# Optimization experiments

Hardware: AMD Instinct MI355X
Metric: run time of the kernel (lower is better)

Reference implementation:

```python
import jax, jax.numpy as jnp
import numpy as np

NUM_FEATURES = 256
NUM_HEADS = 8
HEAD_SIZE = NUM_FEATURES // NUM_HEADS  # 32
N_AGENTS = 8
B = 32
SEQ = 64


def setup_inputs() -> dict:
    key = jax.random.key(0)
    ks = jax.random.split(key, 6)
    s = 0.02
    x = jax.random.normal(ks[0], (N_AGENTS * B, NUM_FEATURES, SEQ), dtype=jnp.float32)
    Wq = jax.random.normal(ks[1], (NUM_HEADS, NUM_FEATURES, HEAD_SIZE), dtype=jnp.float32) * s
    Wk = jax.random.normal(ks[2], (NUM_HEADS, NUM_FEATURES, HEAD_SIZE), dtype=jnp.float32) * s
    Wv = jax.random.normal(ks[3], (NUM_HEADS, NUM_FEATURES, HEAD_SIZE), dtype=jnp.float32) * s
    Wp = jax.random.normal(ks[4], (NUM_FEATURES, NUM_FEATURES), dtype=jnp.float32) * s
    bp = jnp.zeros((NUM_FEATURES,), dtype=jnp.float32)
    return {"x": x, "Wq": Wq, "Wk": Wk, "Wv": Wv, "Wp": Wp, "bp": bp, "n_agents": N_AGENTS}


def reference(x, Wq, Wk, Wv, Wp, bp, n_agents):
    # x: (n_agents*b, f, h)
    b_total, f, h = x.shape
    b = b_total // n_agents
    # reshape + rearrange 'n b f h -> n b h f'  (t = token axis of length h)
    xs = x.reshape(n_agents, b, f, h).transpose(0, 1, 3, 2)  # (n, b, t, f)
    # All heads at once: per-head linear projections (no bias)
    q = jnp.einsum('nbtf,Hfd->Hnbtd', xs, Wq)
    k = jnp.einsum('nbtf,Hfd->Hnbtd', xs, Wk)
    v = jnp.einsum('nbtf,Hfd->Hnbtd', xs, Wv)
    # all-pairs agent attention: i = key agent, j = query agent
    scale = f ** (-0.5)  # source scales by num_features, not head_size
    scores = jnp.einsum('Hjbtd,Hibsd->Hijbts', q, k) * scale  # (H,n,n,b,t,s)
    attn = jax.nn.softmax(scores, axis=-1)
    # weighted values, then sum over key-agent axis i
    out = jnp.einsum('Hijbts,Hibsd->Hjbtd', attn, v)  # (H,n,b,t,d)
    # concat heads on last dim (head 0 first), matching torch.cat
    y = jnp.moveaxis(out, 0, 3).reshape(n_agents, b, h, f)  # (n,b,t,H*d)
    # output projection (dropout is identity at eval / p=0)
    y = jnp.einsum('nbtf,gf->nbtg', y, Wp) + bp
    # rearrange 'n b h f -> n b f h' then merge agents into batch
    y = y.transpose(0, 1, 3, 2).reshape(n_agents * b, f, h)
    return y
```

## Files before the change

kernel.cpp:

```cpp
#include <hip/hip_runtime.h>

#define F   256
#define T   64
#define NH  8
#define D   32
#define NA  8
#define NBB 32

typedef unsigned short ushortT;
typedef unsigned int   uintT;

typedef short bf16x8 __attribute__((ext_vector_type(8)));
typedef float f32x4  __attribute__((ext_vector_type(4)));

__device__ __forceinline__ float bf2f(ushortT u) {
    union { uintT i; float f; } c; c.i = ((uintT)u) << 16; return c.f;
}
__device__ __forceinline__ ushortT f2bf(float f) {
    union { float f; uintT u; } c; c.f = f;
    uintT u = c.u;
    uintT r = u + 0x7fffu + ((u >> 16) & 1u);
    return (ushortT)(r >> 16);
}

__device__ __forceinline__ int detect_isbf16(const void* xraw) {
    const uintT* w = (const uintT*)xraw;
    int bad = 0;
    for (int k = 0; k < 128; ++k) {
        uintT v = w[k];
        uintT e0 = (v >> 7)  & 0xffu;
        uintT e1 = (v >> 23) & 0xffu;
        bad += (e0 > 131u) + (e1 > 131u);
    }
    return bad == 0 ? 1 : 0;
}

__device__ __forceinline__ ushortT cvt_elem(const void* p, size_t i, bool isbf) {
    return isbf ? ((const ushortT*)p)[i] : f2bf(((const float*)p)[i]);
}

__device__ __forceinline__ void packc(const f32x4 v, float scale, uintT& u0, uintT& u1) {
    u0 = (uintT)f2bf(v[0] * scale) | ((uintT)f2bf(v[1] * scale) << 16);
    u1 = (uintT)f2bf(v[2] * scale) | ((uintT)f2bf(v[3] * scale) << 16);
}

__device__ __forceinline__ bf16x8 build_frag(uintT u0a, uintT u1a, uintT u0b, uintT u1b,
                                             int sl0, int sl1, bool hi) {
    union { uintT u[4]; bf16x8 v; } r;
    uintT x0a = (uintT)__shfl((int)u0a, sl0), x0b = (uintT)__shfl((int)u0b, sl0);
    uintT x1a = (uintT)__shfl((int)u1a, sl0), x1b = (uintT)__shfl((int)u1b, sl0);
    uintT x2a = (uintT)__shfl((int)u0a, sl1), x2b = (uintT)__shfl((int)u0b, sl1);
    uintT x3a = (uintT)__shfl((int)u1a, sl1), x3b = (uintT)__shfl((int)u1b, sl1);
    r.u[0] = hi ? x0b : x0a;
    r.u[1] = hi ? x1b : x1a;
    r.u[2] = hi ? x2b : x2a;
    r.u[3] = hi ? x3b : x3a;
    return r.v;
}

__device__ __forceinline__ int xposU(int t, int f) {
    return t * 256 + ((((f >> 3) ^ (t & 31)) * 8) | (f & 7));
}
#define FRAGPOS(t_, ks_, quad_) \
    ((t_) * 256 + ((((4 * (ks_) + (quad_)) ^ ((t_) & 31)) * 8)))

template <int NT>
__device__ __forceinline__ void stage_xT(const void* x, int nb, ushortT* xs,
                                         bool isbf, int tid) {
    int t = tid & 63;
    int g0 = tid >> 6;
    const int GP = NT / 64;
    #pragma unroll
    for (int it = 0; it < 64 / GP; ++it) {
        int g = g0 + it * GP;
        float v0, v1, v2, v3;
        if (isbf) {
            const ushortT* xp = (const ushortT*)x + (size_t)nb * (F * T) + (size_t)g * 4 * T + t;
            v0 = bf2f(xp[0]); v1 = bf2f(xp[T]); v2 = bf2f(xp[2 * T]); v3 = bf2f(xp[3 * T]);
        } else {
            const float* xp = (const float*)x + (size_t)nb * (F * T) + (size_t)g * 4 * T + t;
            v0 = xp[0]; v1 = xp[T]; v2 = xp[2 * T]; v3 = xp[3 * T];
        }
        uintT lo = (uintT)f2bf(v0) | ((uintT)f2bf(v1) << 16);
        uintT hi2 = (uintT)f2bf(v2) | ((uintT)f2bf(v3) << 16);
        *(uint2*)&xs[xposU(t, g * 4)] = make_uint2(lo, hi2);
    }
}


__global__ __launch_bounds__(256) void wprep_kernel(const void* __restrict__ Wq,
                                                    const void* __restrict__ Wk,
                                                    const void* __restrict__ Wv,
                                                    const void* __restrict__ x,
                                                    ushortT* __restrict__ Wt) {
    __shared__ int sflag;
    if (threadIdx.x == 0) sflag = detect_isbf16(x);
    __syncthreads();
    bool isbf = sflag != 0;

    int base = (blockIdx.x * 256 + threadIdx.x) * 8;
    int cp = base >> 8, f0 = base & 255;
    int qkv = cp >> 8, c = cp & 255, hh = c >> 5, d = c & 31;
    const void* W = (qkv == 0) ? Wq : (qkv == 1) ? Wk : Wv;

    ushortT tmp[8];
    #pragma unroll
    for (int jj = 0; jj < 8; ++jj)
        tmp[jj] = cvt_elem(W, (size_t)(hh * F + f0 + jj) * D + d, isbf);
    *(uint4*)&Wt[base] = *(const uint4*)tmp;
}

__global__ __launch_bounds__(256) void qkv_kernel(const void* __restrict__ x,
                                                  const ushortT* __restrict__ Wt,
                                                  ushortT* __restrict__ Kws,
                                                  ushortT* __restrict__ Vws) {
    int nb = blockIdx.x, half = blockIdx.y;
    __shared__ __align__(16) ushortT xs[T * F];
    __shared__ int sflag;
    int tid = threadIdx.x;
    if (tid == 0) sflag = detect_isbf16(x);
    __syncthreads();
    bool isbf = sflag != 0;
    stage_xT<256>(x, nb, xs, isbf, tid);
    __syncthreads();

    int w = tid >> 6, lane = tid & 63, l15 = lane & 15, quad = lane >> 4;
    int rowbase = 256 + 256 * half + 64 * w;

    f32x4 acc[4][4];
    #pragma unroll
    for (int a = 0; a < 4; ++a)
        #pragma unroll
        for (int c = 0; c < 4; ++c) acc[a][c] = (f32x4){0.f, 0.f, 0.f, 0.f};

    #pragma unroll
    for (int ks = 0; ks < 8; ++ks) {
        bf16x8 Bfr[4];
        #pragma unroll
        for (int nt = 0; nt < 4; ++nt) {
            int t = 16 * nt + l15;
            Bfr[nt] = *(const bf16x8*)&xs[FRAGPOS(t, ks, quad)];
        }
        #pragma unroll
        for (int mt = 0; mt < 4; ++mt) {
            bf16x8 Afr = *(const bf16x8*)(Wt +
                (size_t)(rowbase + 16 * mt + l15) * 256 + ks * 32 + quad * 8);
            #pragma unroll
            for (int nt = 0; nt < 4; ++nt)
                acc[mt][nt] = __builtin_amdgcn_mfma_f32_16x16x32_bf16(Afr, Bfr[nt],
                                                                      acc[mt][nt], 0, 0, 0);
        }
    }

    #pragma unroll
    for (int mt = 0; mt < 4; ++mt) {
        int rel = 64 * w + 16 * mt + 4 * quad;
        int hh = rel >> 5, db = rel & 31;
        #pragma unroll
        for (int nt = 0; nt < 4; ++nt) {
            int t = 16 * nt + l15;
            f32x4 v = acc[mt][nt];
            if (half == 0) {
                ushortT* dst = Kws + ((size_t)(nb * NH + hh) * T + t) * D + db;
                uintT lo = (uintT)f2bf(v[0]) | ((uintT)f2bf(v[1]) << 16);
                uintT hi2 = (uintT)f2bf(v[2]) | ((uintT)f2bf(v[3]) << 16);
                *(uint2*)dst = make_uint2(lo, hi2);
            } else {
                #pragma unroll
                for (int r = 0; r < 4; ++r)
                    Vws[((size_t)(nb * NH + hh) * D + db + r) * T + t] = f2bf(v[r]);
            }
        }
    }
}

__global__ __launch_bounds__(512, 2) void attn_kernel(const void* __restrict__ x,
                                                      const ushortT* __restrict__ Wt,
                                                      const ushortT* __restrict__ Kws,
                                                      const ushortT* __restrict__ Vws,
                                                      const void* __restrict__ Wp,
                                                      const void* __restrict__ bp,
                                                      void* __restrict__ outp) {
    __shared__ __align__(16) ushortT xs[T * F];
    __shared__ float bpf[F];
    __shared__ int sflag;

    int tid = threadIdx.x;
    int b = blockIdx.x, j = blockIdx.y;
    int nbj = j * NBB + b;

    if (tid == 0) sflag = detect_isbf16(x);
    __syncthreads();
    bool isbf = sflag != 0;
    stage_xT<512>(x, nbj, xs, isbf, tid);
    if (tid < 256)
        bpf[tid] = isbf ? bf2f(((const ushortT*)bp)[tid]) : ((const float*)bp)[tid];
    __syncthreads();

    int h = tid >> 6, lane = tid & 63, l15 = lane & 15, quad = lane >> 4;
    bool hi = quad >= 2;
    int sl0 = l15 + 32 * (quad & 1), sl1 = sl0 + 16;

    bf16x8 qf[4];
    {
        f32x4 qacc[2][4];
        #pragma unroll
        for (int mt = 0; mt < 2; ++mt)
            #pragma unroll
            for (int nt = 0; nt < 4; ++nt) qacc[mt][nt] = (f32x4){0.f, 0.f, 0.f, 0.f};
        #pragma unroll
        for (int ks = 0; ks < 8; ++ks) {
            bf16x8 xf[4];
            #pragma unroll
            for (int nt = 0; nt < 4; ++nt) {
                int t = 16 * nt + l15;
                xf[nt] = *(const bf16x8*)&xs[FRAGPOS(t, ks, quad)];
            }
            #pragma unroll
            for (int mt = 0; mt < 2; ++mt) {
                bf16x8 Aw = *(const bf16x8*)(Wt +
                    (size_t)(32 * h + 16 * mt + l15) * 256 + ks * 32 + quad * 8);
                #pragma unroll
                for (int nt = 0; nt < 4; ++nt)
                    qacc[mt][nt] = __builtin_amdgcn_mfma_f32_16x16x32_bf16(
                        Aw, xf[nt], qacc[mt][nt], 0, 0, 0);
            }
        }
        #pragma unroll
        for (int tt = 0; tt < 4; ++tt) {
            uintT a0, a1, b0, b1;
            packc(qacc[0][tt], 0.0625f, a0, a1);
            packc(qacc[1][tt], 0.0625f, b0, b1);
            qf[tt] = build_frag(a0, a1, b0, b1, sl0, sl1, hi);
        }
    }

    f32x4 oacc[2][4];
    #pragma unroll
    for (int mt = 0; mt < 2; ++mt)
        #pragma unroll
        for (int tt = 0; tt < 4; ++tt) oacc[mt][tt] = (f32x4){0.f, 0.f, 0.f, 0.f};

    #pragma unroll
    for (int i = 0; i < NA; ++i) {
        int nbi = i * NBB + b;
        const ushortT* Kb = Kws + (size_t)(nbi * NH + h) * T * D;
        const ushortT* Vb = Vws + (size_t)(nbi * NH + h) * D * T;

        bf16x8 kf[4], vf[2][2];
        #pragma unroll
        for (int st = 0; st < 4; ++st)
            kf[st] = *(const bf16x8*)(Kb + (16 * st + l15) * D + quad * 8);
        #pragma unroll
        for (int mt = 0; mt < 2; ++mt)
            #pragma unroll
            for (int kx = 0; kx < 2; ++kx)
                vf[mt][kx] = *(const bf16x8*)(Vb + (16 * mt + l15) * T + kx * 32 + quad * 8);

        float psum[4] = {0.f, 0.f, 0.f, 0.f};
        uintT pu0[4][4], pu1[4][4];
        #pragma unroll
        for (int st = 0; st < 4; ++st) {
            f32x4 s4[4];
            #pragma unroll
            for (int tt = 0; tt < 4; ++tt)
                s4[tt] = __builtin_amdgcn_mfma_f32_16x16x32_bf16(
                    kf[st], qf[tt], (f32x4){0.f, 0.f, 0.f, 0.f}, 0, 0, 0);
            #pragma unroll
            for (int tt = 0; tt < 4; ++tt) {
                #pragma unroll
                for (int r = 0; r < 4; ++r) {
                    float e = __expf(s4[tt][r]);
                    s4[tt][r] = e;
                    psum[tt] += e;
                }
                packc(s4[tt], 1.f, pu0[st][tt], pu1[st][tt]);
            }
        }
        float inv[4];
        #pragma unroll
        for (int tt = 0; tt < 4; ++tt) {
            float s = psum[tt];
            s += __shfl_xor(s, 16);
            s += __shfl_xor(s, 32);
            inv[tt] = 1.0f / s;
        }

        f32x4 pv[2][4];
        #pragma unroll
        for (int mt = 0; mt < 2; ++mt)
            #pragma unroll
            for (int tt = 0; tt < 4; ++tt) pv[mt][tt] = (f32x4){0.f, 0.f, 0.f, 0.f};
        #pragma unroll
        for (int kx = 0; kx < 2; ++kx) {
            #pragma unroll
            for (int tt = 0; tt < 4; ++tt) {
                bf16x8 pf = build_frag(pu0[2 * kx][tt], pu1[2 * kx][tt],
                                       pu0[2 * kx + 1][tt], pu1[2 * kx + 1][tt],
                                       sl0, sl1, hi);
                #pragma unroll
                for (int mt = 0; mt < 2; ++mt)
                    pv[mt][tt] = __builtin_amdgcn_mfma_f32_16x16x32_bf16(
                        vf[mt][kx], pf, pv[mt][tt], 0, 0, 0);
            }
        }
        #pragma unroll
        for (int mt = 0; mt < 2; ++mt)
            #pragma unroll
            for (int tt = 0; tt < 4; ++tt)
                #pragma unroll
                for (int r = 0; r < 4; ++r)
                    oacc[mt][tt][r] = fmaf(inv[tt], pv[mt][tt][r], oacc[mt][tt][r]);
    }

    __syncthreads();
    #pragma unroll
    for (int mt = 0; mt < 2; ++mt)
        #pragma unroll
        for (int tt = 0; tt < 4; ++tt) {
            int t = 16 * tt + l15;
            int cb = 32 * h + 16 * mt + 4 * quad;
            uintT u0, u1;
            packc(oacc[mt][tt], 1.f, u0, u1);
            *(uint2*)&xs[xposU(t, cb)] = make_uint2(u0, u1);
        }
    __syncthreads();

    f32x4 cacc[2][4];
    #pragma unroll
    for (int a = 0; a < 2; ++a)
        #pragma unroll
        for (int c = 0; c < 4; ++c) cacc[a][c] = (f32x4){0.f, 0.f, 0.f, 0.f};

    #pragma unroll
    for (int ks = 0; ks < 8; ++ks) {
        bf16x8 yb[4];
        #pragma unroll
        for (int nt = 0; nt < 4; ++nt) {
            int t = 16 * nt + l15;
            yb[nt] = *(const bf16x8*)&xs[FRAGPOS(t, ks, quad)];
        }
        #pragma unroll
        for (int m2 = 0; m2 < 2; ++m2) {
            int g = 16 * (2 * h + m2) + l15;
            bf16x8 wf;
            if (isbf) {
                wf = *(const bf16x8*)((const ushortT*)Wp + (size_t)g * 256 +
                                      ks * 32 + quad * 8);
            } else {
                const float* wr = (const float*)Wp + (size_t)g * 256 + ks * 32 + quad * 8;
                float4 w0 = *(const float4*)wr;
                float4 w1 = *(const float4*)(wr + 4);
                union { ushortT s[8]; bf16x8 v; } wt;
                wt.s[0] = f2bf(w0.x); wt.s[1] = f2bf(w0.y);
                wt.s[2] = f2bf(w0.z); wt.s[3] = f2bf(w0.w);
                wt.s[4] = f2bf(w1.x); wt.s[5] = f2bf(w1.y);
                wt.s[6] = f2bf(w1.z); wt.s[7] = f2bf(w1.w);
                wf = wt.v;
            }
            #pragma unroll
            for (int nt = 0; nt < 4; ++nt)
                cacc[m2][nt] = __builtin_amdgcn_mfma_f32_16x16x32_bf16(
                    wf, yb[nt], cacc[m2][nt], 0, 0, 0);
        }
    }

    #pragma unroll
    for (int m2 = 0; m2 < 2; ++m2)
        #pragma unroll
        for (int nt = 0; nt < 4; ++nt) {
            int t = 16 * nt + l15;
            #pragma unroll
            for (int r = 0; r < 4; ++r) {
                int g = 16 * (2 * h + m2) + 4 * quad + r;
                float val = cacc[m2][nt][r] + bpf[g];
                if (isbf)
                    ((ushortT*)outp)[(size_t)nbj * F * T + g * T + t] = f2bf(val);
                else
                    ((float*)outp)[(size_t)nbj * F * T + g * T + t] = val;
            }
        }
}

__device__ __forceinline__ float tof(ushortT u) { return bf2f(u); }
__device__ __forceinline__ float tof(float f)   { return f; }

__device__ __forceinline__ void stage_x(const void* x, size_t nb, ushortT* sX,
                                        bool isbf, int tid) {
    if (isbf) {
        const int4* xg = (const int4*)((const ushortT*)x + nb * (F * T));
        int4* xl = (int4*)sX;
        for (int kk = tid; kk < F * T / 8; kk += 512) xl[kk] = xg[kk];
    } else {
        const float4* xg = (const float4*)((const float*)x + nb * (F * T));
        for (int kk = tid; kk < F * T / 4; kk += 512) {
            float4 v = xg[kk];
            int o = kk * 4;
            sX[o + 0] = f2bf(v.x); sX[o + 1] = f2bf(v.y);
            sX[o + 2] = f2bf(v.z); sX[o + 3] = f2bf(v.w);
        }
    }
}

template <typename WT>
__device__ __forceinline__ void q_proj(const WT* __restrict__ W, const ushortT* sX,
                                       ushortT* dst, int c, int t0) {
    float acc[32];
    #pragma unroll
    for (int m = 0; m < 32; ++m) acc[m] = 0.f;
    for (int f = 0; f < F; ++f) {
        float w = tof(W[f * D]);
        const ushortT* xr = &sX[f * T + t0];
        #pragma unroll
        for (int m = 0; m < 32; ++m) acc[m] = fmaf(bf2f(xr[m]), w, acc[m]);
    }
    #pragma unroll
    for (int m = 0; m < 32; ++m) dst[(t0 + m) * F + c] = f2bf(acc[m]);
}

template <typename WT>
__device__ __forceinline__ void kv_proj(const WT* __restrict__ WK, const WT* __restrict__ WV,
                                        const ushortT* sX, ushortT* sK, ushortT* sV,
                                        int c, int t0) {
    float ak[32], av[32];
    #pragma unroll
    for (int m = 0; m < 32; ++m) { ak[m] = 0.f; av[m] = 0.f; }
    for (int f = 0; f < F; ++f) {
        float wk = tof(WK[f * D]);
        float wv = tof(WV[f * D]);
        const ushortT* xr = &sX[f * T + t0];
        #pragma unroll
        for (int m = 0; m < 32; ++m) {
            float xv = bf2f(xr[m]);
            ak[m] = fmaf(xv, wk, ak[m]);
            av[m] = fmaf(xv, wv, av[m]);
        }
    }
    #pragma unroll
    for (int m = 0; m < 32; ++m) {
        sK[(t0 + m) * F + c] = f2bf(ak[m]);
        sV[(t0 + m) * F + c] = f2bf(av[m]);
    }
}

__global__ __launch_bounds__(512) void fused_kernel(const void* __restrict__ x,
                                                    const void* __restrict__ Wq,
                                                    const void* __restrict__ Wk,
                                                    const void* __restrict__ Wv,
                                                    const void* __restrict__ Wp,
                                                    const void* __restrict__ bp,
                                                    void* __restrict__ outp) {
    __shared__ __align__(16) char smem[98304];
    __shared__ int sflag;
    ushortT* sX = (ushortT*)smem;
    ushortT* sK = (ushortT*)(smem + 32768);
    ushortT* sV = (ushortT*)(smem + 65536);
    float*   sO = (float*)smem;

    int tid = threadIdx.x;
    int b = blockIdx.x, j = blockIdx.y;
    size_t nbj = (size_t)j * NBB + b;

    if (tid == 0) sflag = detect_isbf16(x);
    __syncthreads();
    bool isbf = sflag != 0;

    stage_x(x, nbj, sX, isbf, tid);
    __syncthreads();

    int c = tid & 255, t0 = (tid >> 8) * 32;
    int hc = c >> 5, dc = c & 31;
    if (isbf) q_proj((const ushortT*)Wq + (size_t)hc * F * D + dc, sX, sK, c, t0);
    else      q_proj((const float*)Wq   + (size_t)hc * F * D + dc, sX, sK, c, t0);
    __syncthreads();

    int h = tid >> 6, t = tid & 63;
    float q[32], o[32];
    #pragma unroll
    for (int dd = 0; dd < 32; ++dd) { q[dd] = bf2f(sK[t * F + h * D + dd]); o[dd] = 0.f; }

    for (int i = 0; i < NA; ++i) {
        __syncthreads();
        stage_x(x, (size_t)(i * NBB + b), sX, isbf, tid);
        __syncthreads();
        if (isbf) kv_proj((const ushortT*)Wk + (size_t)hc * F * D + dc,
                          (const ushortT*)Wv + (size_t)hc * F * D + dc, sX, sK, sV, c, t0);
        else      kv_proj((const float*)Wk   + (size_t)hc * F * D + dc,
                          (const float*)Wv   + (size_t)hc * F * D + dc, sX, sK, sV, c, t0);
        __syncthreads();
        float l = 0.f;
        float oi[32];
        #pragma unroll
        for (int dd = 0; dd < 32; ++dd) oi[dd] = 0.f;
        for (int s = 0; s < T; ++s) {
            const ushortT* kr = &sK[s * F + h * D];
            float dot = 0.f;
            #pragma unroll
            for (int dd = 0; dd < 32; ++dd) dot = fmaf(q[dd], bf2f(kr[dd]), dot);
            float e = __expf(dot * 0.0625f);
            l += e;
            const ushortT* vr = &sV[s * F + h * D];
            #pragma unroll
            for (int dd = 0; dd < 32; ++dd) oi[dd] = fmaf(e, bf2f(vr[dd]), oi[dd]);
        }
        float inv = 1.0f / l;
        #pragma unroll
        for (int dd = 0; dd < 32; ++dd) o[dd] = fmaf(oi[dd], inv, o[dd]);
    }
    __syncthreads();

    #pragma unroll
    for (int dd = 0; dd < 32; ++dd) sO[(h * D + dd) * T + t] = o[dd];
    __syncthreads();

    {
        int g = tid >> 1, te0 = (tid & 1) * 32;
        float acc[32];
        #pragma unroll
        for (int m = 0; m < 32; ++m) acc[m] = 0.f;
        if (isbf) {
            const ushortT* Wrow = (const ushortT*)Wp + (size_t)g * F;
            for (int cc = 0; cc < F; ++cc) {
                float w = bf2f(Wrow[cc]);
                const float* yr = &sO[cc * T + te0];
                #pragma unroll
                for (int m = 0; m < 32; ++m) acc[m] = fmaf(yr[m], w, acc[m]);
            }
        } else {
            const float* Wrow = (const float*)Wp + (size_t)g * F;
            for (int cc = 0; cc < F; ++cc) {
                float w = Wrow[cc];
                const float* yr = &sO[cc * T + te0];
                #pragma unroll
                for (int m = 0; m < 32; ++m) acc[m] = fmaf(yr[m], w, acc[m]);
            }
        }
        float bias = isbf ? bf2f(((const ushortT*)bp)[g]) : ((const float*)bp)[g];
        if (isbf) {
            ushortT* ob = (ushortT*)outp + nbj * F * T + g * T + te0;
            #pragma unroll
            for (int m = 0; m < 32; ++m) ob[m] = f2bf(acc[m] + bias);
        } else {
            float* ob = (float*)outp + nbj * F * T + g * T + te0;
            #pragma unroll
            for (int m = 0; m < 32; ++m) ob[m] = acc[m] + bias;
        }
    }
}

extern "C" void kernel_launch(void* const* d_in, const int* in_sizes, int n_in,
                              void* d_out, int out_size, void* d_ws, size_t ws_size,
                              hipStream_t stream) {
    const void* x  = d_in[0];
    const void* Wq = d_in[1];
    const void* Wk = d_in[2];
    const void* Wv = d_in[3];
    const void* Wp = d_in[4];
    const void* bp = d_in[5];

    const size_t needA = 17170432;

    if (ws_size >= needA) {
        char* ws = (char*)d_ws;
        ushortT* Wt  = (ushortT*)(ws + 0);
        ushortT* Kws = (ushortT*)(ws + 393216);
        ushortT* Vws = (ushortT*)(ws + 8781824);

        wprep_kernel<<<dim3(96),     dim3(256), 0, stream>>>(Wq, Wk, Wv, x, Wt);
        qkv_kernel  <<<dim3(256, 2), dim3(256), 0, stream>>>(x, Wt, Kws, Vws);
        attn_kernel <<<dim3(32, 8),  dim3(512), 0, stream>>>(x, Wt, Kws, Vws, Wp, bp, d_out);
    } else {
        fused_kernel<<<dim3(32, 8), dim3(512), 0, stream>>>(x, Wq, Wk, Wv, Wp, bp, d_out);
    }
}
```

Measured before the change: 164.2 us.

## Split attention kernel across query-token halves and pre-convert Wp to bf16

```diff
diff --git a/kernel.cpp b/kernel.cpp
--- a/kernel.cpp
+++ b/kernel.cpp
@@ -64,6 +64,37 @@
 #define FRAGPOS(t_, ks_, quad_) \
     ((t_) * 256 + ((((4 * (ks_) + (quad_)) ^ ((t_) & 31)) * 8)))
 
+
+__global__ __launch_bounds__(256) void wprep_kernel(const void* __restrict__ Wq,
+                                                    const void* __restrict__ Wk,
+                                                    const void* __restrict__ Wv,
+                                                    const void* __restrict__ Wp,
+                                                    const void* __restrict__ x,
+                                                    ushortT* __restrict__ Wt) {
+    __shared__ int sflag;
+    if (threadIdx.x == 0) sflag = detect_isbf16(x);
+    __syncthreads();
+    bool isbf = sflag != 0;
+
+    int base = (blockIdx.x * 256 + threadIdx.x) * 8;
+    int cp = base >> 8, f0 = base & 255;
+
+    ushortT tmp[8];
+    if (cp < 768) {
+        int qkv = cp >> 8, c = cp & 255, hh = c >> 5, d = c & 31;
+        const void* W = (qkv == 0) ? Wq : (qkv == 1) ? Wk : Wv;
+        #pragma unroll
+        for (int jj = 0; jj < 8; ++jj)
+            tmp[jj] = cvt_elem(W, (size_t)(hh * F + f0 + jj) * D + d, isbf);
+    } else {
+        int g = cp - 768;
+        #pragma unroll
+        for (int jj = 0; jj < 8; ++jj)
+            tmp[jj] = cvt_elem(Wp, (size_t)g * F + f0 + jj, isbf);
+    }
+    *(uint4*)&Wt[base] = *(const uint4*)tmp;
+}
+
 template <int NT>
 __device__ __forceinline__ void stage_xT(const void* x, int nb, ushortT* xs,
                                          bool isbf, int tid) {
@@ -83,31 +114,8 @@
         }
         uintT lo = (uintT)f2bf(v0) | ((uintT)f2bf(v1) << 16);
         uintT hi2 = (uintT)f2bf(v2) | ((uintT)f2bf(v3) << 16);
-        *(uint2*)&xs[xposU(t, g * 4)] = make_uint2(lo, hi2);
-    }
-}
-
-
-__global__ __launch_bounds__(256) void wprep_kernel(const void* __restrict__ Wq,
-                                                    const void* __restrict__ Wk,
-                                                    const void* __restrict__ Wv,
-                                                    const void* __restrict__ x,
-                                                    ushortT* __restrict__ Wt) {
-    __shared__ int sflag;
-    if (threadIdx.x == 0) sflag = detect_isbf16(x);
-    __syncthreads();
-    bool isbf = sflag != 0;
-
-    int base = (blockIdx.x * 256 + threadIdx.x) * 8;
-    int cp = base >> 8, f0 = base & 255;
-    int qkv = cp >> 8, c = cp & 255, hh = c >> 5, d = c & 31;
-    const void* W = (qkv == 0) ? Wq : (qkv == 1) ? Wk : Wv;
-
-    ushortT tmp[8];
-    #pragma unroll
-    for (int jj = 0; jj < 8; ++jj)
-        tmp[jj] = cvt_elem(W, (size_t)(hh * F + f0 + jj) * D + d, isbf);
-    *(uint4*)&Wt[base] = *(const uint4*)tmp;
+        *(uint2*)&xs[xposU(t & 31, g * 4) + (t >> 5) * 8192] = make_uint2(lo, hi2);
+    }
 }
 
 __global__ __launch_bounds__(256) void qkv_kernel(const void* __restrict__ x,
@@ -139,7 +147,7 @@
         #pragma unroll
         for (int nt = 0; nt < 4; ++nt) {
             int t = 16 * nt + l15;
-            Bfr[nt] = *(const bf16x8*)&xs[FRAGPOS(t, ks, quad)];
+            Bfr[nt] = *(const bf16x8*)&xs[FRAGPOS(t & 31, ks, quad) + (t >> 5) * 8192];
         }
         #pragma unroll
         for (int mt = 0; mt < 4; ++mt) {
@@ -178,21 +186,41 @@
                                                       const ushortT* __restrict__ Wt,
                                                       const ushortT* __restrict__ Kws,
                                                       const ushortT* __restrict__ Vws,
-                                                      const void* __restrict__ Wp,
                                                       const void* __restrict__ bp,
                                                       void* __restrict__ outp) {
-    __shared__ __align__(16) ushortT xs[T * F];
+    __shared__ __align__(16) ushortT xs[32 * F];
     __shared__ float bpf[F];
     __shared__ int sflag;
 
     int tid = threadIdx.x;
-    int b = blockIdx.x, j = blockIdx.y;
+    int b = blockIdx.x, j = blockIdx.y, tb = blockIdx.z;
     int nbj = j * NBB + b;
 
     if (tid == 0) sflag = detect_isbf16(x);
     __syncthreads();
     bool isbf = sflag != 0;
-    stage_xT<512>(x, nbj, xs, isbf, tid);
+
+    {
+        int t = tid & 31, fg = tid >> 5;
+        int ta = tb * 32 + t;
+        #pragma unroll
+        for (int it = 0; it < 4; ++it) {
+            int f0 = (fg + 16 * it) * 4;
+            float v0, v1, v2, v3;
+            if (isbf) {
+                const ushortT* xp = (const ushortT*)x + (size_t)nbj * (F * T) +
+                                    (size_t)f0 * T + ta;
+                v0 = bf2f(xp[0]); v1 = bf2f(xp[T]); v2 = bf2f(xp[2 * T]); v3 = bf2f(xp[3 * T]);
+            } else {
+                const float* xp = (const float*)x + (size_t)nbj * (F * T) +
+                                  (size_t)f0 * T + ta;
+                v0 = xp[0]; v1 = xp[T]; v2 = xp[2 * T]; v3 = xp[3 * T];
+            }
+            uintT lo = (uintT)f2bf(v0) | ((uintT)f2bf(v1) << 16);
+            uintT hi2 = (uintT)f2bf(v2) | ((uintT)f2bf(v3) << 16);
+            *(uint2*)&xs[xposU(t, f0)] = make_uint2(lo, hi2);
+        }
+    }
     if (tid < 256)
         bpf[tid] = isbf ? bf2f(((const ushortT*)bp)[tid]) : ((const float*)bp)[tid];
     __syncthreads();
@@ -201,33 +229,31 @@
     bool hi = quad >= 2;
     int sl0 = l15 + 32 * (quad & 1), sl1 = sl0 + 16;
 
-    bf16x8 qf[4];
+    bf16x8 qf[2];
     {
-        f32x4 qacc[2][4];
+        f32x4 qacc[2][2];
         #pragma unroll
         for (int mt = 0; mt < 2; ++mt)
             #pragma unroll
-            for (int nt = 0; nt < 4; ++nt) qacc[mt][nt] = (f32x4){0.f, 0.f, 0.f, 0.f};
+            for (int nt = 0; nt < 2; ++nt) qacc[mt][nt] = (f32x4){0.f, 0.f, 0.f, 0.f};
         #pragma unroll
         for (int ks = 0; ks < 8; ++ks) {
-            bf16x8 xf[4];
-            #pragma unroll
-            for (int nt = 0; nt < 4; ++nt) {
-                int t = 16 * nt + l15;
-                xf[nt] = *(const bf16x8*)&xs[FRAGPOS(t, ks, quad)];
-            }
+            bf16x8 xf[2];
+            #pragma unroll
+            for (int nt = 0; nt < 2; ++nt)
+                xf[nt] = *(const bf16x8*)&xs[FRAGPOS(16 * nt + l15, ks, quad)];
             #pragma unroll
             for (int mt = 0; mt < 2; ++mt) {
                 bf16x8 Aw = *(const bf16x8*)(Wt +
                     (size_t)(32 * h + 16 * mt + l15) * 256 + ks * 32 + quad * 8);
                 #pragma unroll
-                for (int nt = 0; nt < 4; ++nt)
+                for (int nt = 0; nt < 2; ++nt)
                     qacc[mt][nt] = __builtin_amdgcn_mfma_f32_16x16x32_bf16(
                         Aw, xf[nt], qacc[mt][nt], 0, 0, 0);
             }
         }
         #pragma unroll
-        for (int tt = 0; tt < 4; ++tt) {
+        for (int tt = 0; tt < 2; ++tt) {
             uintT a0, a1, b0, b1;
             packc(qacc[0][tt], 0.0625f, a0, a1);
             packc(qacc[1][tt], 0.0625f, b0, b1);
@@ -235,89 +261,75 @@
         }
     }
 
-    f32x4 oacc[2][4];
+    f32x4 oacc[2][2];
     #pragma unroll
     for (int mt = 0; mt < 2; ++mt)
         #pragma unroll
-        for (int tt = 0; tt < 4; ++tt) oacc[mt][tt] = (f32x4){0.f, 0.f, 0.f, 0.f};
-
-    #pragma unroll
+        for (int tt = 0; tt < 2; ++tt) oacc[mt][tt] = (f32x4){0.f, 0.f, 0.f, 0.f};
+
     for (int i = 0; i < NA; ++i) {
         int nbi = i * NBB + b;
         const ushortT* Kb = Kws + (size_t)(nbi * NH + h) * T * D;
         const ushortT* Vb = Vws + (size_t)(nbi * NH + h) * D * T;
 
-        bf16x8 kf[4], vf[2][2];
-        #pragma unroll
-        for (int st = 0; st < 4; ++st)
-            kf[st] = *(const bf16x8*)(Kb + (16 * st + l15) * D + quad * 8);
+        float psum[2] = {0.f, 0.f};
+        f32x4 pv[2][2];
         #pragma unroll
         for (int mt = 0; mt < 2; ++mt)
             #pragma unroll
-            for (int kx = 0; kx < 2; ++kx)
-                vf[mt][kx] = *(const bf16x8*)(Vb + (16 * mt + l15) * T + kx * 32 + quad * 8);
-
-        float psum[4] = {0.f, 0.f, 0.f, 0.f};
-        uintT pu0[4][4], pu1[4][4];
-        #pragma unroll
-        for (int st = 0; st < 4; ++st) {
-            f32x4 s4[4];
-            #pragma unroll
-            for (int tt = 0; tt < 4; ++tt)
-                s4[tt] = __builtin_amdgcn_mfma_f32_16x16x32_bf16(
-                    kf[st], qf[tt], (f32x4){0.f, 0.f, 0.f, 0.f}, 0, 0, 0);
-            #pragma unroll
-            for (int tt = 0; tt < 4; ++tt) {
+            for (int tt = 0; tt < 2; ++tt) pv[mt][tt] = (f32x4){0.f, 0.f, 0.f, 0.f};
+
+        #pragma unroll
+        for (int kx = 0; kx < 2; ++kx) {
+            uintT pu0[2][2], pu1[2][2];
+            #pragma unroll
+            for (int sp = 0; sp < 2; ++sp) {
+                bf16x8 kf = *(const bf16x8*)(Kb + (16 * (2 * kx + sp) + l15) * D + quad * 8);
                 #pragma unroll
-                for (int r = 0; r < 4; ++r) {
-                    float e = __expf(s4[tt][r]);
-                    s4[tt][r] = e;
-                    psum[tt] += e;
+                for (int tt = 0; tt < 2; ++tt) {
+                    f32x4 s4 = __builtin_amdgcn_mfma_f32_16x16x32_bf16(
+                        kf, qf[tt], (f32x4){0.f, 0.f, 0.f, 0.f}, 0, 0, 0);
+                    #pragma unroll
+                    for (int r = 0; r < 4; ++r) {
+                        float e = __expf(s4[r]);
+                        s4[r] = e;
+                        psum[tt] += e;
+                    }
+                    packc(s4, 1.f, pu0[sp][tt], pu1[sp][tt]);
                 }
-                packc(s4[tt], 1.f, pu0[st][tt], pu1[st][tt]);
-            }
-        }
-        float inv[4];
-        #pragma unroll
-        for (int tt = 0; tt < 4; ++tt) {
+            }
+            bf16x8 vf0 = *(const bf16x8*)(Vb + l15 * T + kx * 32 + quad * 8);
+            bf16x8 vf1 = *(const bf16x8*)(Vb + (16 + l15) * T + kx * 32 + quad * 8);
+            #pragma unroll
+            for (int tt = 0; tt < 2; ++tt) {
+                bf16x8 pf = build_frag(pu0[0][tt], pu1[0][tt], pu0[1][tt], pu1[1][tt],
+                                       sl0, sl1, hi);
+                pv[0][tt] = __builtin_amdgcn_mfma_f32_16x16x32_bf16(
+                    vf0, pf, pv[0][tt], 0, 0, 0);
+                pv[1][tt] = __builtin_amdgcn_mfma_f32_16x16x32_bf16(
+                    vf1, pf, pv[1][tt], 0, 0, 0);
+            }
+        }
+
+        #pragma unroll
+        for (int tt = 0; tt < 2; ++tt) {
             float s = psum[tt];
             s += __shfl_xor(s, 16);
             s += __shfl_xor(s, 32);
-            inv[tt] = 1.0f / s;
-        }
-
-        f32x4 pv[2][4];
-        #pragma unroll
-        for (int mt = 0; mt < 2; ++mt)
-            #pragma unroll
-            for (int tt = 0; tt < 4; ++tt) pv[mt][tt] = (f32x4){0.f, 0.f, 0.f, 0.f};
-        #pragma unroll
-        for (int kx = 0; kx < 2; ++kx) {
-            #pragma unroll
-            for (int tt = 0; tt < 4; ++tt) {
-                bf16x8 pf = build_frag(pu0[2 * kx][tt], pu1[2 * kx][tt],
-                                       pu0[2 * kx + 1][tt], pu1[2 * kx + 1][tt],
-                                       sl0, sl1, hi);
-                #pragma unroll
-                for (int mt = 0; mt < 2; ++mt)
-                    pv[mt][tt] = __builtin_amdgcn_mfma_f32_16x16x32_bf16(
-                        vf[mt][kx], pf, pv[mt][tt], 0, 0, 0);
-            }
-        }
-        #pragma unroll
-        for (int mt = 0; mt < 2; ++mt)
-            #pragma unroll
-            for (int tt = 0; tt < 4; ++tt)
+            float inv = 1.0f / s;
+            #pragma unroll
+            for (int mt = 0; mt < 2; ++mt)
                 #pragma unroll
                 for (int r = 0; r < 4; ++r)
-                    oacc[mt][tt][r] = fmaf(inv[tt], pv[mt][tt][r], oacc[mt][tt][r]);
+                    oacc[mt][tt][r] = fmaf(inv, pv[mt][tt][r], oacc[mt][tt][r]);
+        }
     }
 
     __syncthreads();
     #pragma unroll
     for (int mt = 0; mt < 2; ++mt)
         #pragma unroll
-        for (int tt = 0; tt < 4; ++tt) {
+        for (int tt = 0; tt < 2; ++tt) {
             int t = 16 * tt + l15;
             int cb = 32 * h + 16 * mt + 4 * quad;
             uintT u0, u1;
@@ -326,40 +338,24 @@
         }
     __syncthreads();
 
-    f32x4 cacc[2][4];
+    f32x4 cacc[2][2];
     #pragma unroll
     for (int a = 0; a < 2; ++a)
         #pragma unroll
-        for (int c = 0; c < 4; ++c) cacc[a][c] = (f32x4){0.f, 0.f, 0.f, 0.f};
+        for (int c = 0; c < 2; ++c) cacc[a][c] = (f32x4){0.f, 0.f, 0.f, 0.f};
 
     #pragma unroll
     for (int ks = 0; ks < 8; ++ks) {
-        bf16x8 yb[4];
-        #pragma unroll
-        for (int nt = 0; nt < 4; ++nt) {
-            int t = 16 * nt + l15;
-            yb[nt] = *(const bf16x8*)&xs[FRAGPOS(t, ks, quad)];
-        }
+        bf16x8 yb[2];
+        #pragma unroll
+        for (int nt = 0; nt < 2; ++nt)
+            yb[nt] = *(const bf16x8*)&xs[FRAGPOS(16 * nt + l15, ks, quad)];
         #pragma unroll
         for (int m2 = 0; m2 < 2; ++m2) {
             int g = 16 * (2 * h + m2) + l15;
-            bf16x8 wf;
-            if (isbf) {
-                wf = *(const bf16x8*)((const ushortT*)Wp + (size_t)g * 256 +
-                                      ks * 32 + quad * 8);
-            } else {
-                const float* wr = (const float*)Wp + (size_t)g * 256 + ks * 32 + quad * 8;
-                float4 w0 = *(const float4*)wr;
-                float4 w1 = *(const float4*)(wr + 4);
-                union { ushortT s[8]; bf16x8 v; } wt;
-                wt.s[0] = f2bf(w0.x); wt.s[1] = f2bf(w0.y);
-                wt.s[2] = f2bf(w0.z); wt.s[3] = f2bf(w0.w);
-                wt.s[4] = f2bf(w1.x); wt.s[5] = f2bf(w1.y);
-                wt.s[6] = f2bf(w1.z); wt.s[7] = f2bf(w1.w);
-                wf = wt.v;
-            }
-            #pragma unroll
-            for (int nt = 0; nt < 4; ++nt)
+            bf16x8 wf = *(const bf16x8*)(Wt + (size_t)(768 + g) * 256 + ks * 32 + quad * 8);
+            #pragma unroll
+            for (int nt = 0; nt < 2; ++nt)
                 cacc[m2][nt] = __builtin_amdgcn_mfma_f32_16x16x32_bf16(
                     wf, yb[nt], cacc[m2][nt], 0, 0, 0);
         }
@@ -368,8 +364,8 @@
     #pragma unroll
     for (int m2 = 0; m2 < 2; ++m2)
         #pragma unroll
-        for (int nt = 0; nt < 4; ++nt) {
-            int t = 16 * nt + l15;
+        for (int nt = 0; nt < 2; ++nt) {
+            int t = tb * 32 + 16 * nt + l15;
             #pragma unroll
             for (int r = 0; r < 4; ++r) {
                 int g = 16 * (2 * h + m2) + 4 * quad + r;
@@ -505,7 +501,7 @@
         }
         float inv = 1.0f / l;
         #pragma unroll
-        for (int dd = 0; dd < 32; ++dd) o[dd] = fmaf(oi[dd], inv, o[dd]);
+        for (int dd = 0; dd < 32; ++dd) o[dd] = fmaf(inv, oi[dd], o[dd]);
     }
     __syncthreads();
 
@@ -558,17 +554,17 @@
     const void* Wp = d_in[4];
     const void* bp = d_in[5];
 
-    const size_t needA = 17170432;
+    const size_t needA = 17301504;
 
     if (ws_size >= needA) {
         char* ws = (char*)d_ws;
         ushortT* Wt  = (ushortT*)(ws + 0);
-        ushortT* Kws = (ushortT*)(ws + 393216);
-        ushortT* Vws = (ushortT*)(ws + 8781824);
-
-        wprep_kernel<<<dim3(96),     dim3(256), 0, stream>>>(Wq, Wk, Wv, x, Wt);
-        qkv_kernel  <<<dim3(256, 2), dim3(256), 0, stream>>>(x, Wt, Kws, Vws);
-        attn_kernel <<<dim3(32, 8),  dim3(512), 0, stream>>>(x, Wt, Kws, Vws, Wp, bp, d_out);
+        ushortT* Kws = (ushortT*)(ws + 524288);
+        ushortT* Vws = (ushortT*)(ws + 8912896);
+
+        wprep_kernel<<<dim3(128),      dim3(256), 0, stream>>>(Wq, Wk, Wv, Wp, x, Wt);
+        qkv_kernel  <<<dim3(256, 2),   dim3(256), 0, stream>>>(x, Wt, Kws, Vws);
+        attn_kernel <<<dim3(32, 8, 2), dim3(512), 0, stream>>>(x, Wt, Kws, Vws, bp, d_out);
     } else {
         fused_kernel<<<dim3(32, 8), dim3(512), 0, stream>>>(x, Wq, Wk, Wv, Wp, bp, d_out);
     }
```

Measured after the change: 150.5 us. 1.09x faster.
